# Kernel optimization log

Measured on AMD Instinct MI355X. Metric: run time of the kernel, lower is better.

## Reference

```python
import jax, jax.numpy as jnp
import numpy as np

C = 256          # embed_dim
NH = 8           # n_heads
NL = 4           # n_levels
NP = 4           # n_points
HD = C // NH     # head dim = 32
SS = np.array([[128, 128], [64, 64], [32, 32], [16, 16]], dtype=np.int64)  # (H_l, W_l)
LSI = np.concatenate([[0], np.cumsum(SS[:, 0] * SS[:, 1])[:-1]]).astype(np.int64)
LIN = int((SS[:, 0] * SS[:, 1]).sum())  # 21760
B = 2
LQ = LIN


def setup_inputs() -> dict:
    key = jax.random.key(0)
    ks = jax.random.split(key, 8)
    s = 0.02
    return {
        "query": jax.random.normal(ks[0], (B, LQ, C), jnp.float32),
        "reference_points": jax.random.uniform(ks[1], (B, LQ, NL, 2), dtype=jnp.float32),
        "input_flatten": jax.random.normal(ks[2], (B, LIN, C), jnp.float32),
        "W_value": jax.random.normal(ks[3], (C, C), jnp.float32) * s,
        "b_value": jnp.zeros((C,), jnp.float32),
        "W_off": jax.random.normal(ks[4], (C, NH * NL * NP * 2), jnp.float32) * s,
        "b_off": jnp.zeros((NH * NL * NP * 2,), jnp.float32),
        "W_attn": jax.random.normal(ks[5], (C, NH * NL * NP), jnp.float32) * s,
        "b_attn": jnp.zeros((NH * NL * NP,), jnp.float32),
        "W_out": jax.random.normal(ks[6], (C, C), jnp.float32) * s,
        "b_out": jnp.zeros((C,), jnp.float32),
        "input_spatial_shapes": jnp.asarray(SS),
        "input_level_start_index": jnp.asarray(LSI),
    }


def _msda(query, reference_points, input_flatten,
          W_value, b_value, W_off, b_off, W_attn, b_attn, W_out, b_out):
    N, Lq, _ = query.shape
    Lin = input_flatten.shape[1]
    # projections
    value = (input_flatten @ W_value + b_value).reshape(N, Lin, NH, HD)
    off = (query @ W_off + b_off).reshape(N, Lq, NH, NL, NP, 2)
    aw = jax.nn.softmax((query @ W_attn + b_attn).reshape(N, Lq, NH, NL * NP), axis=-1)
    aw = aw.reshape(N, Lq, NH, NL, NP)
    # normalizer is (W_l, H_l) per level
    norm = jnp.asarray(SS[:, ::-1].copy(), jnp.float32)  # (NL, 2)
    loc = reference_points[:, :, None, :, None, :] + off / norm[None, None, None, :, None, :]
    out = jnp.zeros((N, Lq, NH, HD), query.dtype)
    for l in range(NL):
        Hl, Wl = int(SS[l, 0]), int(SS[l, 1])
        st = int(LSI[l])
        v = value[:, st:st + Hl * Wl].transpose(0, 2, 1, 3)  # (N, NH, HW, HD)
        # grid_sample align_corners=False semantics: pixel = loc*size - 0.5
        x = loc[:, :, :, l, :, 0] * Wl - 0.5  # (N, Lq, NH, NP)
        y = loc[:, :, :, l, :, 1] * Hl - 0.5
        x0 = jnp.floor(x)
        y0 = jnp.floor(y)
        lw = x - x0
        lh = y - y0
        x0i = x0.astype(jnp.int32)
        y0i = y0.astype(jnp.int32)

        def corner(ix, iy, w):
            valid = (ix >= 0) & (ix < Wl) & (iy >= 0) & (iy < Hl)
            idx = jnp.clip(iy * Wl + ix, 0, Hl * Wl - 1)
            idx_t = idx.transpose(0, 2, 1, 3).reshape(N, NH, Lq * NP)
            g = jnp.take_along_axis(v, idx_t[:, :, :, None], axis=2)
            g = g.reshape(N, NH, Lq, NP, HD)
            wt = (w * valid).transpose(0, 2, 1, 3)  # (N, NH, Lq, NP)
            return g * wt[..., None]

        samp = (corner(x0i, y0i, (1 - lw) * (1 - lh))
                + corner(x0i + 1, y0i, lw * (1 - lh))
                + corner(x0i, y0i + 1, (1 - lw) * lh)
                + corner(x0i + 1, y0i + 1, lw * lh))
        out = out + jnp.einsum('nhqpd,nqhp->nqhd', samp, aw[:, :, :, l])
    return out.reshape(N, Lq, C) @ W_out + b_out


def reference(query, reference_points, input_flatten,
              W_value, b_value, W_off, b_off, W_attn, b_attn, W_out, b_out,
              input_spatial_shapes, input_level_start_index):
    return _msda(query, reference_points, input_flatten,
                 W_value, b_value, W_off, b_off, W_attn, b_attn, W_out, b_out)
```

## Files before the change

kernel.cpp:

```cpp
#include <hip/hip_runtime.h>

typedef unsigned short u16;
typedef unsigned int u32;
typedef short bf16x8 __attribute__((ext_vector_type(8)));
typedef float f32x4 __attribute__((ext_vector_type(4)));

#define LQ_ 21760
#define LIN_ 21760
#define CDIM 256
#define MROWS (2 * LQ_)

__device__ __forceinline__ u16 f2bf(float f) {
  u32 u;
  __builtin_memcpy(&u, &f, 4);
  u32 r = (u + 0x7fffu + ((u >> 16) & 1u)) >> 16;
  return (u16)r;
}
__device__ __forceinline__ u32 pack_bf16_rne(float a, float b) {
  return (u32)f2bf(a) | ((u32)f2bf(b) << 16);
}
__device__ __forceinline__ float bflo(u32 u) {
  u32 v = u << 16;
  float f;
  __builtin_memcpy(&f, &v, 4);
  return f;
}
__device__ __forceinline__ float bfhi(u32 u) {
  u32 v = u & 0xffff0000u;
  float f;
  __builtin_memcpy(&f, &v, 4);
  return f;
}

__device__ __forceinline__ void conv_one(const float* W0, const float* W1, u16* Wf,
                                         int N, int split, int blk, int t) {
  const int tid = blk * 256 + t;
  if (tid >= N * 32) return;
  const int n = tid >> 5, kcg = tid & 31;
  float w[8];
#pragma unroll
  for (int j = 0; j < 8; ++j) {
    const int k = kcg * 8 + j;
    w[j] = (n < split) ? W0[(size_t)k * split + n]
                       : W1[(size_t)k * (N - split) + (n - split)];
  }
  uint4 pk;
  pk.x = pack_bf16_rne(w[0], w[1]);
  pk.y = pack_bf16_rne(w[2], w[3]);
  pk.z = pack_bf16_rne(w[4], w[5]);
  pk.w = pack_bf16_rne(w[6], w[7]);
  const int ks = kcg >> 2, kcr = kcg & 3, c = n >> 4;
  const int chunk = ks * (N / 4) + c * 4 + kcr;
  *(uint4*)(Wf + (size_t)chunk * 128 + (n & 15) * 8) = pk;
}

__global__ __launch_bounds__(256) void conv_fused(
    const float* __restrict__ Wv, const float* __restrict__ Wof,
    const float* __restrict__ Wa, const float* __restrict__ Wo,
    const float* __restrict__ bof, const float* __restrict__ ba,
    u16* __restrict__ WfV, u16* __restrict__ WfC, u16* __restrict__ WfO,
    float* __restrict__ bcat, const float* __restrict__ Aq,
    const float* __restrict__ Ai, u16* __restrict__ Qf, u16* __restrict__ If) {
  const int b = blockIdx.x, t = threadIdx.x;
  if (b < 32) {
    conv_one(Wv, Wv, WfV, 256, 256, b, t);
    return;
  }
  if (b < 80) {
    conv_one(Wof, Wa, WfC, 384, 256, b - 32, t);
    return;
  }
  if (b < 112) {
    conv_one(Wo, Wo, WfO, 256, 256, b - 80, t);
    return;
  }
  if (b < 114) {
    const int i = (b - 112) * 256 + t;
    if (i < 384) bcat[i] = (i < 256) ? bof[i] : ba[i - 256];
    return;
  }
  const int i = (b - 114) * 256 + t;
  const int n4 = MROWS * 32;
  const float* src;
  u16* dst;
  int j;
  if (i < n4) {
    src = Aq;
    dst = Qf;
    j = i;
  } else {
    src = Ai;
    dst = If;
    j = i - n4;
  }
  const int tile = j >> 9;
  const int c2 = (j >> 4) & 31;
  const int sr = j & 15;
  const int row = (tile >> 3) * 128 + (c2 >> 2) * 16 + sr;
  const int kc = (tile & 7) * 32 + (c2 & 3) * 8;
  const float4 f0 = *(const float4*)(src + (size_t)row * 256 + kc);
  const float4 f1 = *(const float4*)(src + (size_t)row * 256 + kc + 4);
  uint4 pk;
  pk.x = pack_bf16_rne(f0.x, f0.y);
  pk.y = pack_bf16_rne(f0.z, f0.w);
  pk.z = pack_bf16_rne(f1.x, f1.y);
  pk.w = pack_bf16_rne(f1.z, f1.w);
  *(uint4*)(dst + (size_t)j * 8) = pk;
}

__global__ __launch_bounds__(256) void gemm_vq(
    const u16* __restrict__ If, const u16* __restrict__ WfV,
    const float* __restrict__ bv, u16* __restrict__ outV,
    const u16* __restrict__ Qf, const u16* __restrict__ WfC,
    const float* __restrict__ bcat, float* __restrict__ outO,
    float* __restrict__ outA) {
  const int t = threadIdx.x, l = t & 63, wv = t >> 6;
  const int wr = wv >> 1, wc = wv & 1;
  const int fq = l >> 4, fr = l & 15;
  bf16x8 af[8][4];

  if (blockIdx.x < 340) {
    const int rb = blockIdx.x;
    const u16* ab = If + (size_t)rb * 32768 + (wr * 16 + fq) * 128 + fr * 8;
#pragma unroll
    for (int ks = 0; ks < 8; ++ks)
#pragma unroll
      for (int r = 0; r < 4; ++r)
        af[ks][r] = *(const bf16x8*)(ab + ks * 4096 + r * 512);
#pragma unroll
    for (int cb = 0; cb < 2; ++cb) {
      f32x4 acc[4][4];
#pragma unroll
      for (int r = 0; r < 4; ++r)
#pragma unroll
        for (int c = 0; c < 4; ++c) acc[r][c] = f32x4{0.f, 0.f, 0.f, 0.f};
      const u16* bb = WfV + ((size_t)(cb * 8 + wc * 4) * 4 + fq) * 128 + fr * 8;
#pragma unroll
      for (int ks = 0; ks < 8; ++ks) {
        bf16x8 bf[4];
#pragma unroll
        for (int c = 0; c < 4; ++c) bf[c] = *(const bf16x8*)(bb + ks * 8192 + c * 512);
#pragma unroll
        for (int c = 0; c < 4; ++c)
#pragma unroll
          for (int r = 0; r < 4; ++r)
            acc[r][c] = __builtin_amdgcn_mfma_f32_16x16x32_bf16(af[ks][r], bf[c],
                                                                acc[r][c], 0, 0, 0);
      }
      const int rq = fq * 4;
#pragma unroll
      for (int c = 0; c < 4; ++c) {
        const int col = cb * 128 + wc * 64 + c * 16 + fr;
        const float bz = bv[col];
#pragma unroll
        for (int r = 0; r < 4; ++r) {
          const int row0 = rb * 128 + wr * 64 + r * 16 + rq;
#pragma unroll
          for (int g = 0; g < 4; ++g)
            outV[(size_t)(row0 + g) * 256 + col] = f2bf(acc[r][c][g] + bz);
        }
      }
    }
  } else {
    const int rb = blockIdx.x - 340;
    const u16* ab = Qf + (size_t)rb * 32768 + (wr * 16 + fq) * 128 + fr * 8;
#pragma unroll
    for (int ks = 0; ks < 8; ++ks)
#pragma unroll
      for (int r = 0; r < 4; ++r)
        af[ks][r] = *(const bf16x8*)(ab + ks * 4096 + r * 512);
#pragma unroll
    for (int cb = 0; cb < 3; ++cb) {
      f32x4 acc[4][4];
#pragma unroll
      for (int r = 0; r < 4; ++r)
#pragma unroll
        for (int c = 0; c < 4; ++c) acc[r][c] = f32x4{0.f, 0.f, 0.f, 0.f};
      const u16* bb = WfC + ((size_t)(cb * 8 + wc * 4) * 4 + fq) * 128 + fr * 8;
#pragma unroll
      for (int ks = 0; ks < 8; ++ks) {
        bf16x8 bf[4];
#pragma unroll
        for (int c = 0; c < 4; ++c) bf[c] = *(const bf16x8*)(bb + ks * 12288 + c * 512);
#pragma unroll
        for (int c = 0; c < 4; ++c)
#pragma unroll
          for (int r = 0; r < 4; ++r)
            acc[r][c] = __builtin_amdgcn_mfma_f32_16x16x32_bf16(af[ks][r], bf[c],
                                                                acc[r][c], 0, 0, 0);
      }
      const int rq = fq * 4;
#pragma unroll
      for (int c = 0; c < 4; ++c) {
        const int col = cb * 128 + wc * 64 + c * 16 + fr;
        const float bz = bcat[col];
#pragma unroll
        for (int r = 0; r < 4; ++r) {
          const int row0 = rb * 128 + wr * 64 + r * 16 + rq;
#pragma unroll
          for (int g = 0; g < 4; ++g) {
            const float v = acc[r][c][g] + bz;
            if (col < 256)
              outO[(size_t)(row0 + g) * 256 + col] = v;
            else
              outA[(size_t)(row0 + g) * 128 + (col - 256)] = v;
          }
        }
      }
    }
  }
}

__global__ __launch_bounds__(256) void gemm_out(
    const u16* __restrict__ A, const u16* __restrict__ Wf,
    const float* __restrict__ bias, float* __restrict__ out) {
  const int rb = blockIdx.x;
  const int t = threadIdx.x, l = t & 63, wv = t >> 6;
  const int wr = wv >> 1, wc = wv & 1;
  const int fq = l >> 4, fr = l & 15;
  bf16x8 af[8][4];
  const u16* ab = A + ((size_t)rb * 128 + wr * 64 + fr) * 256 + fq * 8;
#pragma unroll
  for (int ks = 0; ks < 8; ++ks)
#pragma unroll
    for (int r = 0; r < 4; ++r)
      af[ks][r] = *(const bf16x8*)(ab + (size_t)r * 4096 + ks * 32);
#pragma unroll
  for (int cb = 0; cb < 2; ++cb) {
    f32x4 acc[4][4];
#pragma unroll
    for (int r = 0; r < 4; ++r)
#pragma unroll
      for (int c = 0; c < 4; ++c) acc[r][c] = f32x4{0.f, 0.f, 0.f, 0.f};
    const u16* bb = Wf + ((size_t)(cb * 8 + wc * 4) * 4 + fq) * 128 + fr * 8;
#pragma unroll
    for (int ks = 0; ks < 8; ++ks) {
      bf16x8 bf[4];
#pragma unroll
      for (int c = 0; c < 4; ++c) bf[c] = *(const bf16x8*)(bb + ks * 8192 + c * 512);
#pragma unroll
      for (int c = 0; c < 4; ++c)
#pragma unroll
        for (int r = 0; r < 4; ++r)
          acc[r][c] = __builtin_amdgcn_mfma_f32_16x16x32_bf16(af[ks][r], bf[c],
                                                              acc[r][c], 0, 0, 0);
    }
    const int rq = fq * 4;
#pragma unroll
    for (int c = 0; c < 4; ++c) {
      const int col = cb * 128 + wc * 64 + c * 16 + fr;
      const float bz = bias[col];
#pragma unroll
      for (int r = 0; r < 4; ++r) {
        const int row0 = rb * 128 + wr * 64 + r * 16 + rq;
#pragma unroll
        for (int g = 0; g < 4; ++g)
          out[(size_t)(row0 + g) * 256 + col] = acc[r][c][g] + bz;
      }
    }
  }
}

__global__ __launch_bounds__(256, 4) void msda_sample5(
    const u16* __restrict__ value, const float* __restrict__ off,
    const float* __restrict__ attnl, const float* __restrict__ refp,
    u16* __restrict__ out) {
  __shared__ float s_aw[64 * 17];
  __shared__ ushort4 s_idx[16 * 64];
  __shared__ float4 s_w[16 * 64];
  const int t = threadIdx.x;
  const int bq0 = blockIdx.x * 8;

  if (t < 64) {
    const float* lg = attnl + (size_t)(bq0 + (t >> 3)) * 128 + (t & 7) * 16;
    float e[16];
    float m = -1e30f;
#pragma unroll
    for (int i = 0; i < 16; ++i) {
      e[i] = lg[i];
      m = fmaxf(m, e[i]);
    }
    float s = 0.f;
#pragma unroll
    for (int i = 0; i < 16; ++i) {
      e[i] = __expf(e[i] - m);
      s += e[i];
    }
    const float inv = 1.f / s;
#pragma unroll
    for (int i = 0; i < 16; ++i) s_aw[t * 17 + i] = e[i] * inv;
  }
  __syncthreads();

#pragma unroll
  for (int rr = 0; rr < 4; ++rr) {
    const int id = t + rr * 256;
    const int qh = id & 63, lp = id >> 6;
    const int q = qh >> 3, h = qh & 7, lv = lp >> 2, p = lp & 3;
    const int bq = bq0 + q;
    const int Wl = 128 >> lv;
    const int st = (lv == 0) ? 0 : (lv == 1) ? 16384 : (lv == 2) ? 20480 : 21504;
    const float ox = off[(size_t)bq * 256 + ((h * 4 + lv) * 4 + p) * 2];
    const float oy = off[(size_t)bq * 256 + ((h * 4 + lv) * 4 + p) * 2 + 1];
    const float rx = refp[(size_t)bq * 8 + lv * 2];
    const float ry = refp[(size_t)bq * 8 + lv * 2 + 1];
    const float aw = s_aw[qh * 17 + lp];
    const float x = rx * (float)Wl + ox - 0.5f;
    const float y = ry * (float)Wl + oy - 0.5f;
    const float xf = floorf(x), yf = floorf(y);
    const int x0 = (int)xf, y0 = (int)yf;
    const float lw = x - xf, lh = y - yf;
    const float hw = 1.f - lw, hh = 1.f - lh;
    const int ixs[4] = {x0, x0 + 1, x0, x0 + 1};
    const int iys[4] = {y0, y0, y0 + 1, y0 + 1};
    const float wts[4] = {hw * hh, lw * hh, hw * lh, lw * lh};
    u32 rows[4];
    float ws4[4];
#pragma unroll
    for (int c = 0; c < 4; ++c) {
      const int ix = ixs[c], iy = iys[c];
      const bool valid = (ix >= 0) & (ix < Wl) & (iy >= 0) & (iy < Wl);
      int idx = iy * Wl + ix;
      idx = max(0, min(idx, Wl * Wl - 1));
      rows[c] = (u32)(st + idx);
      ws4[c] = valid ? (wts[c] * aw) : 0.f;
    }
    ushort4 iv;
    iv.x = (u16)rows[0];
    iv.y = (u16)rows[1];
    iv.z = (u16)rows[2];
    iv.w = (u16)rows[3];
    s_idx[lp * 64 + qh] = iv;
    s_w[lp * 64 + qh] = make_float4(ws4[0], ws4[1], ws4[2], ws4[3]);
  }
  __syncthreads();

  const int q = t >> 5, h = (t >> 2) & 7, dg = t & 3;
  const int qh = q * 8 + h;
  const int bq = bq0 + q;
  const u16* vp = value + (size_t)((bq >= LQ_) ? LIN_ : 0) * CDIM + h * 32 + dg * 8;
  float a0 = 0.f, a1 = 0.f, a2 = 0.f, a3 = 0.f;
  float a4 = 0.f, a5 = 0.f, a6 = 0.f, a7 = 0.f;
#pragma unroll
  for (int lp = 0; lp < 16; ++lp) {
    const ushort4 iv = s_idx[lp * 64 + qh];
    const float4 wv = s_w[lp * 64 + qh];
    const u32 rows[4] = {iv.x, iv.y, iv.z, iv.w};
    const float ww[4] = {wv.x, wv.y, wv.z, wv.w};
#pragma unroll
    for (int c = 0; c < 4; ++c) {
      const uint4 d = *(const uint4*)(vp + (size_t)rows[c] * CDIM);
      const float w = ww[c];
      a0 += w * bflo(d.x);
      a1 += w * bfhi(d.x);
      a2 += w * bflo(d.y);
      a3 += w * bfhi(d.y);
      a4 += w * bflo(d.z);
      a5 += w * bfhi(d.z);
      a6 += w * bflo(d.w);
      a7 += w * bfhi(d.w);
    }
  }
  uint4 o;
  o.x = pack_bf16_rne(a0, a1);
  o.y = pack_bf16_rne(a2, a3);
  o.z = pack_bf16_rne(a4, a5);
  o.w = pack_bf16_rne(a6, a7);
  *(uint4*)(out + (size_t)bq * CDIM + h * 32 + dg * 8) = o;
}

extern "C" void kernel_launch(void* const* d_in, const int* in_sizes, int n_in,
                              void* d_out, int out_size, void* d_ws, size_t ws_size,
                              hipStream_t stream) {
  const float* query = (const float*)d_in[0];
  const float* refp = (const float*)d_in[1];
  const float* inflat = (const float*)d_in[2];
  const float* Wv = (const float*)d_in[3];
  const float* bv = (const float*)d_in[4];
  const float* Wof = (const float*)d_in[5];
  const float* bof = (const float*)d_in[6];
  const float* Wa = (const float*)d_in[7];
  const float* ba = (const float*)d_in[8];
  const float* Wo = (const float*)d_in[9];
  const float* bo = (const float*)d_in[10];
  float* out = (float*)d_out;

  const size_t M = MROWS;

  u16* If = (u16*)d_ws;
  u16* Qf = If + M * 256;
  u16* ws_value = Qf + M * 256;
  float* ws_off = (float*)(ws_value + M * 256);
  float* ws_attn = ws_off + M * 256;
  u16* WfV = (u16*)(ws_attn + M * 128);
  u16* WfC = WfV + 256 * 256;
  u16* WfO = WfC + 384 * 256;
  float* bcat = (float*)(WfO + 256 * 256);
  u16* ws_samp = If;

  conv_fused<<<dim3(10994), dim3(256), 0, stream>>>(Wv, Wof, Wa, Wo, bof, ba, WfV, WfC,
                                                    WfO, bcat, query, inflat, Qf, If);
  gemm_vq<<<dim3(680), dim3(256), 0, stream>>>(If, WfV, bv, ws_value, Qf, WfC, bcat,
                                               ws_off, ws_attn);
  msda_sample5<<<dim3(5440), dim3(256), 0, stream>>>(ws_value, ws_off, ws_attn, refp,
                                                     ws_samp);
  gemm_out<<<dim3(340), dim3(256), 0, stream>>>(ws_samp, WfO, bo, out);
}
```

Baseline: 294.0 us.

## Stream A fragments per k-step instead of preloading, raise GEMM occupancy

The GEMM kernels no longer preload the full 8x4 A-fragment array into registers. They reload four fragments per k-step inside each column-block pass, and an asm barrier stops the compiler from hoisting those loads back out. Launch bounds now request 4 blocks per SM so fewer VGPRs are used and more waves can hide latency. The conversion kernel now writes Q/I in plain row-major bf16 instead of a pre-tiled layout, which matches the new row-major A loads. The cost is re-reading A from global/L2 once per column block, and the row-major fragment loads are strided.

```diff
diff --git a/kernel.cpp b/kernel.cpp
--- a/kernel.cpp
+++ b/kernel.cpp
@@ -93,13 +93,8 @@
     dst = If;
     j = i - n4;
   }
-  const int tile = j >> 9;
-  const int c2 = (j >> 4) & 31;
-  const int sr = j & 15;
-  const int row = (tile >> 3) * 128 + (c2 >> 2) * 16 + sr;
-  const int kc = (tile & 7) * 32 + (c2 & 3) * 8;
-  const float4 f0 = *(const float4*)(src + (size_t)row * 256 + kc);
-  const float4 f1 = *(const float4*)(src + (size_t)row * 256 + kc + 4);
+  const float4 f0 = *(const float4*)(src + (size_t)j * 8);
+  const float4 f1 = *(const float4*)(src + (size_t)j * 8 + 4);
   uint4 pk;
   pk.x = pack_bf16_rne(f0.x, f0.y);
   pk.y = pack_bf16_rne(f0.z, f0.w);
@@ -108,7 +103,7 @@
   *(uint4*)(dst + (size_t)j * 8) = pk;
 }
 
-__global__ __launch_bounds__(256) void gemm_vq(
+__global__ __launch_bounds__(256, 4) void gemm_vq(
     const u16* __restrict__ If, const u16* __restrict__ WfV,
     const float* __restrict__ bv, u16* __restrict__ outV,
     const u16* __restrict__ Qf, const u16* __restrict__ WfC,
@@ -117,18 +112,15 @@
   const int t = threadIdx.x, l = t & 63, wv = t >> 6;
   const int wr = wv >> 1, wc = wv & 1;
   const int fq = l >> 4, fr = l & 15;
-  bf16x8 af[8][4];
 
   if (blockIdx.x < 340) {
     const int rb = blockIdx.x;
-    const u16* ab = If + (size_t)rb * 32768 + (wr * 16 + fq) * 128 + fr * 8;
-#pragma unroll
-    for (int ks = 0; ks < 8; ++ks)
-#pragma unroll
-      for (int r = 0; r < 4; ++r)
-        af[ks][r] = *(const bf16x8*)(ab + ks * 4096 + r * 512);
+    const u16* ab = If + ((size_t)(rb * 128 + wr * 64 + fr)) * 256 + fq * 8;
 #pragma unroll
     for (int cb = 0; cb < 2; ++cb) {
+      int zz = 0;
+      asm volatile("" : "+v"(zz));
+      const u16* abx = ab + zz;
       f32x4 acc[4][4];
 #pragma unroll
       for (int r = 0; r < 4; ++r)
@@ -137,6 +129,10 @@
       const u16* bb = WfV + ((size_t)(cb * 8 + wc * 4) * 4 + fq) * 128 + fr * 8;
 #pragma unroll
       for (int ks = 0; ks < 8; ++ks) {
+        bf16x8 af[4];
+#pragma unroll
+        for (int r = 0; r < 4; ++r)
+          af[r] = *(const bf16x8*)(abx + (size_t)r * 4096 + ks * 32);
         bf16x8 bf[4];
 #pragma unroll
         for (int c = 0; c < 4; ++c) bf[c] = *(const bf16x8*)(bb + ks * 8192 + c * 512);
@@ -144,7 +140,7 @@
         for (int c = 0; c < 4; ++c)
 #pragma unroll
           for (int r = 0; r < 4; ++r)
-            acc[r][c] = __builtin_amdgcn_mfma_f32_16x16x32_bf16(af[ks][r], bf[c],
+            acc[r][c] = __builtin_amdgcn_mfma_f32_16x16x32_bf16(af[r], bf[c],
                                                                 acc[r][c], 0, 0, 0);
       }
       const int rq = fq * 4;
@@ -163,14 +159,12 @@
     }
   } else {
     const int rb = blockIdx.x - 340;
-    const u16* ab = Qf + (size_t)rb * 32768 + (wr * 16 + fq) * 128 + fr * 8;
-#pragma unroll
-    for (int ks = 0; ks < 8; ++ks)
-#pragma unroll
-      for (int r = 0; r < 4; ++r)
-        af[ks][r] = *(const bf16x8*)(ab + ks * 4096 + r * 512);
+    const u16* ab = Qf + ((size_t)(rb * 128 + wr * 64 + fr)) * 256 + fq * 8;
 #pragma unroll
     for (int cb = 0; cb < 3; ++cb) {
+      int zz = 0;
+      asm volatile("" : "+v"(zz));
+      const u16* abx = ab + zz;
       f32x4 acc[4][4];
 #pragma unroll
       for (int r = 0; r < 4; ++r)
@@ -179,6 +173,10 @@
       const u16* bb = WfC + ((size_t)(cb * 8 + wc * 4) * 4 + fq) * 128 + fr * 8;
 #pragma unroll
       for (int ks = 0; ks < 8; ++ks) {
+        bf16x8 af[4];
+#pragma unroll
+        for (int r = 0; r < 4; ++r)
+          af[r] = *(const bf16x8*)(abx + (size_t)r * 4096 + ks * 32);
         bf16x8 bf[4];
 #pragma unroll
         for (int c = 0; c < 4; ++c) bf[c] = *(const bf16x8*)(bb + ks * 12288 + c * 512);
@@ -186,7 +184,7 @@
         for (int c = 0; c < 4; ++c)
 #pragma unroll
           for (int r = 0; r < 4; ++r)
-            acc[r][c] = __builtin_amdgcn_mfma_f32_16x16x32_bf16(af[ks][r], bf[c],
+            acc[r][c] = __builtin_amdgcn_mfma_f32_16x16x32_bf16(af[r], bf[c],
                                                                 acc[r][c], 0, 0, 0);
       }
       const int rq = fq * 4;
@@ -211,22 +209,19 @@
   }
 }
 
-__global__ __launch_bounds__(256) void gemm_out(
+__global__ __launch_bounds__(256, 4) void gemm_out(
     const u16* __restrict__ A, const u16* __restrict__ Wf,
     const float* __restrict__ bias, float* __restrict__ out) {
   const int rb = blockIdx.x;
   const int t = threadIdx.x, l = t & 63, wv = t >> 6;
   const int wr = wv >> 1, wc = wv & 1;
   const int fq = l >> 4, fr = l & 15;
-  bf16x8 af[8][4];
   const u16* ab = A + ((size_t)rb * 128 + wr * 64 + fr) * 256 + fq * 8;
 #pragma unroll
-  for (int ks = 0; ks < 8; ++ks)
-#pragma unroll
-    for (int r = 0; r < 4; ++r)
-      af[ks][r] = *(const bf16x8*)(ab + (size_t)r * 4096 + ks * 32);
-#pragma unroll
   for (int cb = 0; cb < 2; ++cb) {
+    int zz = 0;
+    asm volatile("" : "+v"(zz));
+    const u16* abx = ab + zz;
     f32x4 acc[4][4];
 #pragma unroll
     for (int r = 0; r < 4; ++r)
@@ -235,6 +230,10 @@
     const u16* bb = Wf + ((size_t)(cb * 8 + wc * 4) * 4 + fq) * 128 + fr * 8;
 #pragma unroll
     for (int ks = 0; ks < 8; ++ks) {
+      bf16x8 af[4];
+#pragma unroll
+      for (int r = 0; r < 4; ++r)
+        af[r] = *(const bf16x8*)(abx + (size_t)r * 4096 + ks * 32);
       bf16x8 bf[4];
 #pragma unroll
       for (int c = 0; c < 4; ++c) bf[c] = *(const bf16x8*)(bb + ks * 8192 + c * 512);
@@ -242,7 +241,7 @@
       for (int c = 0; c < 4; ++c)
 #pragma unroll
         for (int r = 0; r < 4; ++r)
-          acc[r][c] = __builtin_amdgcn_mfma_f32_16x16x32_bf16(af[ks][r], bf[c],
+          acc[r][c] = __builtin_amdgcn_mfma_f32_16x16x32_bf16(af[r], bf[c],
                                                               acc[r][c], 0, 0, 0);
     }
     const int rq = fq * 4;
```

After: 339.2 us. +15.4%, slower.
